# Kernel tuning notes

Hardware: AMD Instinct MI355X
Metric: run time of the kernel (lower is better)

## Reference

```python
import jax, jax.numpy as jnp
import numpy as np

# ---- fixed physiological constants (match init_kwargs cell/synapse params) ----
DT = 0.1  # ms
N_CELL_TYPES = 2
S_REC, S_FF, S_TOT = 3, 1, 4
TAU_MEM = jnp.array([20.0, 10.0])
THETA = jnp.array([-50.0, -50.0])
U_RESET = jnp.array([-65.0, -65.0])
E_L = jnp.array([-70.0, -70.0])
G_L = jnp.array([10.0, 10.0])
TAU_REF_STEPS = jnp.round(jnp.array([2.0, 1.0]) / DT)  # [20, 10] steps
# combined recurrent(3) + FF(1) synapse channels
TAU_RISE = jnp.array([0.5, 2.0, 0.5, 0.5])
TAU_DECAY = jnp.array([2.0, 100.0, 5.0, 2.0])
E_SYN = jnp.array([0.0, 0.0, -80.0, 0.0])
G_BAR = jnp.array([1.0, 0.5, 1.0, 1.0])
SYN2CELL = jnp.array([0, 0, 1])  # recurrent synapse -> presynaptic cell type
A_RISE = jnp.exp(-DT / TAU_RISE)
A_DECAY = jnp.exp(-DT / TAU_DECAY)


def spike(x):
    return (x > 0).astype(x.dtype)


def setup_inputs() -> dict:
    key = jax.random.key(0)
    ks = jax.random.split(key, 8)
    N, NI, B, T = 4096, 1024, 8, 500
    ci = jax.random.randint(ks[0], (N,), 0, 2).astype(jnp.int32)  # 0=exc, 1=inh
    ci_ff = jnp.zeros((NI,), dtype=jnp.int32)
    # sparse signed recurrent weights (Dale's law: sign by presynaptic type)
    mag = jnp.abs(jax.random.normal(ks[1], (N, N))) * 0.02
    sign = jnp.where(ci == 1, -1.0, 1.0)[:, None]
    mask = jax.random.bernoulli(ks[2], 0.1, (N, N))
    weights = (mag * sign * mask).astype(jnp.float32)
    # sparse positive feedforward weights
    mag_ff = jnp.abs(jax.random.normal(ks[3], (NI, N))) * 0.05
    mask_ff = jax.random.bernoulli(ks[4], 0.2, (NI, N))
    weights_FF = (mag_ff * mask_ff).astype(jnp.float32)
    scaling_factors = jax.random.uniform(ks[5], (2, 2), minval=0.5, maxval=1.5)
    scaling_factors_FF = jax.random.uniform(ks[6], (1, 2), minval=0.5, maxval=1.5)
    input_spikes = (jax.random.uniform(ks[7], (B, T, NI)) < 0.05).astype(jnp.float32)
    return {
        "input_spikes": input_spikes,
        "weights": weights,
        "weights_FF": weights_FF,
        "scaling_factors": scaling_factors,
        "scaling_factors_FF": scaling_factors_FF,
        "cell_type_indices": ci,
        "cell_type_indices_FF": ci_ff,
    }


def reference(input_spikes, weights, weights_FF, scaling_factors, scaling_factors_FF,
              cell_type_indices, cell_type_indices_FF):
    ci = cell_type_indices
    B, T, NI = input_spikes.shape
    N = weights.shape[0]
    # per-neuron parameter gathers
    tau_mem = TAU_MEM[ci]
    theta = THETA[ci]
    u_reset = U_RESET[ci]
    e_l = E_L[ci]
    g_l = G_L[ci]
    ref_steps = TAU_REF_STEPS[ci]
    # cell-type pairwise scaling applied to (masked) weights
    W_eff = weights * scaling_factors[ci[:, None], ci[None, :]]            # (N,N)
    Wff_eff = weights_FF * scaling_factors_FF[cell_type_indices_FF[:, None], ci[None, :]]
    cell_masks = jnp.stack([(ci == c).astype(weights.dtype) for c in range(N_CELL_TYPES)])  # (2,N)
    # precompute feedforward synaptic drive for all timesteps: (T,B,N)
    drive_ff = jnp.einsum('bti,ij->tbj', input_spikes, Wff_eff) * G_BAR[S_REC]

    v0 = jnp.broadcast_to(e_l, (B, N))
    h0 = jnp.zeros((B, N, S_TOT), weights.dtype)
    g0 = jnp.zeros((B, N, S_TOT), weights.dtype)
    ref0 = jnp.zeros((B, N), weights.dtype)
    s0 = jnp.zeros((B, N), weights.dtype)

    def step(carry, dff_t):
        v, h, g, ref, s_prev = carry
        # recurrent drive split by presynaptic cell type, routed to synapse channels
        drive_c = jnp.stack([(s_prev * cell_masks[c]) @ W_eff for c in range(N_CELL_TYPES)], axis=-1)  # (B,N,2)
        drive_rec = drive_c[..., SYN2CELL] * G_BAR[:S_REC]                  # (B,N,3)
        drive = jnp.concatenate([drive_rec, dff_t[..., None]], axis=-1)    # (B,N,4)
        # double-exponential conductance kinetics
        h = h * A_RISE + drive
        g = g * A_DECAY + (1.0 - A_DECAY) * h
        # conductance-based membrane update
        I_syn = jnp.sum(g * (E_SYN - v[..., None]), axis=-1)                # (B,N)
        v_new = v + (DT / tau_mem) * ((e_l - v) + I_syn / g_l)
        refr = (ref > 0).astype(v.dtype)
        v_new = refr * u_reset + (1.0 - refr) * v_new
        s_new = spike(v_new - theta) * (1.0 - refr)
        spk = s_new > 0.5
        v_post = jnp.where(spk, u_reset, v_new)
        ref_new = jnp.where(spk, ref_steps, jnp.maximum(ref - 1.0, 0.0))
        return (v_post, h, g, ref_new, s_new), s_new

    _, spikes = jax.lax.scan(step, (v0, h0, g0, ref0, s0), drive_ff)
    return jnp.transpose(spikes, (1, 0, 2))  # (B,T,N)
```

## Files before the change

### kernel.cpp

```cpp
#include <hip/hip_runtime.h>
#include <cstdint>
#include <cstddef>

#define N_NEU   4096
#define N_IN    1024
#define B_SZ    8
#define T_STEPS 500
#define NSLICE  16
#define NBLK    (B_SZ * NSLICE)
#define FF_WORDS (B_SZ * T_STEPS * 16)
#define FFP_STRIDE 33
#define FFP_CAP 128
#define N_PAIRS (B_SZ * T_STEPS)

#define WS_TM_OFF    0
#define WS_MB_OFF    512
#define WS_FFM_OFF   17408
#define WS_FFD_OFF   529408
#define WS_FLN_OFF   66065408
#define WS_FL_OFF    66081792
#define WS_NEED_FFD  (529408 + (size_t)T_STEPS * B_SZ * N_NEU * 4)
#define WS_NEED_FL   (66081792 + (size_t)N_PAIRS * FFP_CAP * 4)

__global__ __launch_bounds__(64) void snn_init(const int* __restrict__ ci,
                                               unsigned long long* __restrict__ tmask,
                                               unsigned long long* __restrict__ mb2) {
    const int k = blockIdx.x, l = threadIdx.x;
    unsigned long long m = __ballot(ci[(k << 6) + l] == 0);
    if (l == 0) tmask[k] = m;
    const int idx = (k << 6) + l;
    if (idx < 2048) mb2[idx] = 0ULL;
}

__global__ __launch_bounds__(256) void snn_ffmask(const float* __restrict__ inspk,
                                                  unsigned long long* __restrict__ ffmask) {
    int gid = blockIdx.x * 256 + threadIdx.x;
    int wid = gid >> 6, lane = gid & 63;
    int nw  = (gridDim.x * 256) >> 6;
    for (int w = wid; w < FF_WORDS; w += nw) {
        float v = inspk[(size_t)w * 64 + lane];
        unsigned long long m = __ballot(v > 0.5f);
        if (lane == 0) ffmask[w] = m;
    }
}

__device__ __forceinline__ int extract_pad(unsigned long long m,
                                           unsigned long long tm_exc,
                                           int* lds, int lane) {
    int pc  = __popcll(m);
    int sum = pc;
#pragma unroll
    for (int d = 1; d < 64; d <<= 1) {
        int o = __shfl_up(sum, d, 64);
        if (lane >= d) sum += o;
    }
    int off   = sum - pc;
    int total = __shfl(sum, 63, 64);
    int base  = lane << 6;
    while (m) {
        int bit = __builtin_ctzll(m);
        int ty  = ((tm_exc >> bit) & 1ULL) ? 0 : 1;
        lds[off++] = ((base + bit) << 2) | ty;
        m &= m - 1ULL;
    }
    int padcnt = (-total) & 63;
    if (lane < padcnt) lds[total + lane] = 2;
    return total;
}

__device__ __forceinline__ int extract_cap(unsigned long long m,
                                           int* buf, int lane) {
    int pc  = __popcll(m);
    int sum = pc;
#pragma unroll
    for (int d = 1; d < 64; d <<= 1) {
        int o = __shfl_up(sum, d, 64);
        if (lane >= d) sum += o;
    }
    int off   = sum - pc;
    int total = __shfl(sum, 63, 64);
    int base  = lane << 6;
    while (m) {
        int bit = __builtin_ctzll(m);
        if (off < FFP_CAP) buf[off] = (base + bit) << 2;
        ++off;
        m &= m - 1ULL;
    }
    if (total < FFP_CAP) {
        int padcnt = (-total) & 63;
        if (lane < padcnt && total + lane < FFP_CAP)
            buf[total + lane] = 2;
    }
    return total;
}

__global__ __launch_bounds__(256) void snn_fflist(
    const unsigned long long* __restrict__ ffmask,
    int* __restrict__ fflist,
    int* __restrict__ fflist_n)
{
    const int lane = threadIdx.x & 63;
    const int wv   = threadIdx.x >> 6;
    const int w    = blockIdx.x * 4 + wv;
    for (int q = 0; q < 4; ++q) {
        const int p = w * 4 + q;
        const int t = p >> 3, b = p & 7;
        const unsigned long long mf =
            (lane < 16) ? ffmask[((size_t)b * T_STEPS + t) * 16 + lane] : 0ULL;
        const int n = extract_cap(mf, fflist + (size_t)p * FFP_CAP, lane);
        if (lane == 0) fflist_n[p] = n;
    }
}

__device__ __forceinline__ void gather2(const int* __restrict__ lst, int npad,
                                        const float* __restrict__ base,
                                        float se, float si,
                                        float* oe, float* oi) {
#pragma clang fp contract(off)
    float ae = 0.0f, ai = 0.0f;
    const int4* lst4 = (const int4*)lst;
    for (int k = 0; k < npad; k += 64) {
        int4  eq[16];
        int   e[64];
        float w[64];
#pragma unroll
        for (int u = 0; u < 16; ++u) eq[u] = lst4[(k >> 2) + u];
#pragma unroll
        for (int u = 0; u < 16; ++u) {
            e[4 * u + 0] = eq[u].x; e[4 * u + 1] = eq[u].y;
            e[4 * u + 2] = eq[u].z; e[4 * u + 3] = eq[u].w;
        }
#pragma unroll
        for (int u = 0; u < 64; ++u) w[u] = base[(size_t)(e[u] >> 2) << 12];
#pragma unroll
        for (int u = 0; u < 64; ++u) {
            const int ty = e[u] & 3;
            const float sc = (ty == 0) ? se : ((ty == 1) ? si : 0.0f);
            const float p  = w[u] * sc;
            ae = (ty == 0) ? ae + p : ae;
            ai = (ty == 1) ? ai + p : ai;
        }
    }
    *oe = ae; *oi = ai;
}

__device__ __forceinline__ float ffp_fold_g(const int* __restrict__ lst, int npad,
                                            const float* __restrict__ lwff,
                                            int j, float sff) {
#pragma clang fp contract(off)
    float acc = 0.0f;
    const int4* l4 = (const int4*)lst;
    for (int k = 0; k < npad; k += 64) {
        int4  eq[16];
        int   e[64];
        float w[64];
#pragma unroll
        for (int u = 0; u < 16; ++u) eq[u] = l4[(k >> 2) + u];
#pragma unroll
        for (int u = 0; u < 16; ++u) {
            e[4 * u + 0] = eq[u].x; e[4 * u + 1] = eq[u].y;
            e[4 * u + 2] = eq[u].z; e[4 * u + 3] = eq[u].w;
        }
#pragma unroll
        for (int u = 0; u < 64; ++u) w[u] = lwff[(e[u] >> 2) * FFP_STRIDE + j];
#pragma unroll
        for (int u = 0; u < 64; ++u) {
            const float sc = ((e[u] & 3) == 0) ? sff : 0.0f;
            const float p  = w[u] * sc;
            acc += p;
        }
    }
    return acc;
}

__global__ __launch_bounds__(512) void snn_ffpre4(
    const unsigned long long* __restrict__ ffmask,
    const float* __restrict__ Wff,
    const float* __restrict__ sfff,
    const int*   __restrict__ ci,
    const int*   __restrict__ fflist,
    const int*   __restrict__ fflist_n,
    float*       __restrict__ ffdrive)
{
#pragma clang fp contract(off)
    const int tid = threadIdx.x;
    const int s   = blockIdx.x & 127;
    const int tbh = blockIdx.x >> 7;
    __shared__ float lwff[N_IN * FFP_STRIDE];

    {
        const int j  = tid & 31;
        const int r0 = tid >> 5;
        for (int r = r0; r < N_IN; r += 16)
            lwff[r * FFP_STRIDE + j] = Wff[(size_t)r * N_NEU + (s << 5) + j];
    }
    __syncthreads();

    const int lane = tid & 63;
    const int wv   = tid >> 6;
    const int j    = lane & 31;
    const int h    = lane >> 5;
    const int jg   = (s << 5) + j;
    const float sff = sfff[ci[jg]];

    for (int k = 0; k < 125; ++k) {
        const int p0 = tbh * 2000 + (((k << 3) | wv) << 1);
        const int p  = p0 + h;
        const int nf = fflist_n[p];
        float acc;
        if (nf <= FFP_CAP) {
            acc = ffp_fold_g(fflist + (size_t)p * FFP_CAP,
                             (nf + 63) & ~63, lwff, j, sff);
        } else {
            const int t = p >> 3, b = p & 7;
            acc = 0.0f;
            const unsigned long long* mp =
                ffmask + ((size_t)b * T_STEPS + t) * 16;
            for (int w16 = 0; w16 < 16; ++w16) {
                unsigned long long mw = mp[w16];
                const int base = w16 << 6;
                while (mw) {
                    const int bit = __builtin_ctzll(mw); mw &= mw - 1ULL;
                    const float pr = lwff[(base + bit) * FFP_STRIDE + j] * sff;
                    acc += pr;
                }
            }
        }
        ffdrive[(size_t)p * N_NEU + jg] = acc;
    }
}

__global__ __launch_bounds__(64) void snn_ffpre(const unsigned long long* __restrict__ ffmask,
                                                const float* __restrict__ Wff,
                                                const float* __restrict__ sfff,
                                                const int*   __restrict__ ci,
                                                float*       __restrict__ ffdrive) {
#pragma clang fp contract(off)
    const int lane  = threadIdx.x;
    const int chunk = blockIdx.x & 63;
    const int tile  = blockIdx.x >> 6;
    const int i     = (chunk << 6) + lane;
    const float s_ff = sfff[ci[i]];
    __shared__ alignas(16) int lds_f[N_IN + 64];
    for (int p = tile * 25; p < tile * 25 + 25; ++p) {
        const int t = p >> 3, b = p & 7;
        const unsigned long long mf =
            (lane < 16) ? ffmask[((size_t)b * T_STEPS + t) * 16 + lane] : 0ULL;
        const int n = extract_pad(mf, ~0ULL, lds_f, lane);
        float fd, dummy;
        gather2(lds_f, (n + 63) & ~63, Wff + i, s_ff, 0.0f, &fd, &dummy);
        ffdrive[((size_t)t * B_SZ + b) * N_NEU + i] = fd;
    }
}

__global__ __launch_bounds__(256) void snn_run(
    const float* __restrict__ W,
    const float* __restrict__ Wff,
    const float* __restrict__ sf,
    const float* __restrict__ sfff,
    const int*   __restrict__ ci,
    float*       __restrict__ out,
    const unsigned long long* __restrict__ ffmask,
    const unsigned long long* __restrict__ tmask_g,
    const float* __restrict__ ffdrive,
    int use_ffpre,
    unsigned long long* __restrict__ mb2)
{
#pragma clang fp contract(off)
    const int tid   = threadIdx.x;
    const int lane  = tid & 63;
    const int wv    = tid >> 6;
    const int bid   = blockIdx.x;
    const int slice = (((bid >> 6) & 1) << 3) | (bid & 7);
    const int b     = (bid >> 3) & 7;
    const int i     = (slice << 8) + (wv << 6) + lane;
    const int c     = ci[i];

    const float s_exc = sf[c];
    const float s_inh = sf[2 + c];
    const float s_ff  = sfff[c];

    const unsigned long long my_tm = tmask_g[lane];

    __shared__ alignas(16) int lds_c[4][N_NEU + 64];
    __shared__ alignas(16) int lds_f[4][N_IN + 64];
    int* const my_ldsc = lds_c[wv];
    int* const my_ldsf = lds_f[wv];

    unsigned long long* const mbB = mb2 + (size_t)b * 128;

    float v = -70.0f, rf = 0.0f;
    float h0 = 0.0f, h1 = 0.0f, h2 = 0.0f, h3 = 0.0f;
    float g0 = 0.0f, g1 = 0.0f, g2 = 0.0f, g3 = 0.0f;

    const float aR0 = expf(-0.1f / 0.5f);
    const float aR1 = expf(-0.1f / 2.0f);
    const float aD0 = expf(-0.1f / 2.0f);
    const float aD1 = expf(-0.1f / 100.0f);
    const float aD2 = expf(-0.1f / 5.0f);
    const float kmem   = c ? (0.1f / 10.0f) : (0.1f / 20.0f);
    const float rsteps = c ? 10.0f : 20.0f;

    const float* const wseg = W + (size_t)((slice << 8) + (wv << 6));

    for (int t = 0; t < T_STEPS; ++t) {
        float ffd = 0.0f;
        if (use_ffpre) {
            ffd = ffdrive[((size_t)t * B_SZ + b) * N_NEU + i];
            asm volatile("" :: "v"(ffd));
        }

        unsigned long long mw = 0ULL;
        if (t > 0) {
            const unsigned int tg = (unsigned int)t;
            const unsigned long long* ep =
                mbB + (size_t)(t & 1) * 1024 + ((size_t)lane << 1);
            unsigned long long w0, w1;
            for (;;) {
                w0 = __hip_atomic_load(&ep[0], __ATOMIC_RELAXED,
                                       __HIP_MEMORY_SCOPE_AGENT);
                w1 = __hip_atomic_load(&ep[1], __ATOMIC_RELAXED,
                                       __HIP_MEMORY_SCOPE_AGENT);
                const bool ok = ((unsigned int)(w0 >> 32) == tg) &&
                                ((unsigned int)(w1 >> 32) == tg);
                if (__ballot(ok) == ~0ULL) break;
                __builtin_amdgcn_s_sleep(1);
            }
            mw = (w0 & 0xFFFFFFFFULL) | ((w1 & 0xFFFFFFFFULL) << 32);
            asm volatile("" ::: "memory");
        }

        {
            unsigned long long mm = mw;
            float wacc = 0.0f;
            const size_t rowbase = (size_t)lane << 18;
            while (mm) {
                const int bit = __builtin_ctzll(mm); mm &= mm - 1ULL;
                const float* r = wseg + rowbase + ((size_t)bit << 12);
                wacc += r[0]; wacc += r[16]; wacc += r[32]; wacc += r[48];
            }
            asm volatile("" :: "v"(wacc));
        }

        int ne = 0;
        if (__ballot(mw != 0ULL) != 0ULL)
            ne = extract_pad(mw, my_tm, my_ldsc, lane);

        if (!use_ffpre) {
            const unsigned long long mf =
                (lane < 16) ? ffmask[((size_t)b * T_STEPS + t) * 16 + lane] : 0ULL;
            const int nf = extract_pad(mf, ~0ULL, my_ldsf, lane);
            float fd, dummy;
            gather2(my_ldsf, (nf + 63) & ~63, Wff + i, s_ff, 0.0f, &fd, &dummy);
            ffd = fd;
        }

        float exc, inh;
        gather2(my_ldsc, (ne + 63) & ~63, W + i, s_exc, s_inh, &exc, &inh);

        const float d0 = exc;
        const float d1 = 0.5f * exc;
        const float d2 = inh;
        const float d3 = ffd;

        h0 = fmaf(h0, aR0, d0);
        h1 = fmaf(h1, aR1, d1);
        h2 = fmaf(h2, aR0, d2);
        h3 = fmaf(h3, aR0, d3);
        g0 = fmaf(g0, aD0, (1.0f - aD0) * h0);
        g1 = fmaf(g1, aD1, (1.0f - aD1) * h1);
        g2 = fmaf(g2, aD2, (1.0f - aD2) * h2);
        g3 = fmaf(g3, aD0, (1.0f - aD0) * h3);

        const float p0 = g0 * (0.0f - v);
        const float p1 = g1 * (0.0f - v);
        const float p2 = g2 * (-80.0f - v);
        const float p3 = g3 * (0.0f - v);
        const float Isyn = ((p0 + p1) + p2) + p3;

        float vn = fmaf(kmem, (-70.0f - v) + Isyn / 10.0f, v);
        const bool refr = rf > 0.0f;
        if (refr) vn = -65.0f;
        const float sn = (!refr && (vn > -50.0f)) ? 1.0f : 0.0f;
        const bool spk = sn > 0.5f;

        const unsigned long long sm = __ballot(spk);
        if (lane == 0) {
            const unsigned long long tg =
                (unsigned long long)(unsigned int)(t + 1) << 32;
            unsigned long long* pp = mb2 + (size_t)((t + 1) & 1) * 1024
                                   + (size_t)b * 128
                                   + ((size_t)((slice << 2) | wv) << 1);
            __hip_atomic_store(&pp[0], tg | (sm & 0xFFFFFFFFULL),
                               __ATOMIC_RELAXED, __HIP_MEMORY_SCOPE_AGENT);
            __hip_atomic_store(&pp[1], tg | (sm >> 32),
                               __ATOMIC_RELAXED, __HIP_MEMORY_SCOPE_AGENT);
        }

        v  = spk ? -65.0f : vn;
        rf = spk ? rsteps : fmaxf(rf - 1.0f, 0.0f);
        out[((size_t)b * T_STEPS + t) * N_NEU + i] = sn;
    }
}

extern "C" void kernel_launch(void* const* d_in, const int* in_sizes, int n_in,
                              void* d_out, int out_size, void* d_ws, size_t ws_size,
                              hipStream_t stream) {
    const float* inspk = (const float*)d_in[0];
    const float* W     = (const float*)d_in[1];
    const float* Wff   = (const float*)d_in[2];
    const float* sf    = (const float*)d_in[3];
    const float* sfff  = (const float*)d_in[4];
    const int*   ci    = (const int*)d_in[5];

    float* out = (float*)d_out;
    unsigned long long* tmask    = (unsigned long long*)((char*)d_ws + WS_TM_OFF);
    unsigned long long* mb2      = (unsigned long long*)((char*)d_ws + WS_MB_OFF);
    unsigned long long* ffmask   = (unsigned long long*)((char*)d_ws + WS_FFM_OFF);
    float*              ffdrive  = (float*)((char*)d_ws + WS_FFD_OFF);
    int*                fflist_n = (int*)((char*)d_ws + WS_FLN_OFF);
    int*                fflist   = (int*)((char*)d_ws + WS_FL_OFF);

    const int use_fl    = (ws_size >= WS_NEED_FL) ? 1 : 0;
    const int use_ffpre = (ws_size >= WS_NEED_FFD) ? 1 : 0;

    snn_init<<<64, 64, 0, stream>>>(ci, tmask, mb2);
    snn_ffmask<<<1000, 256, 0, stream>>>(inspk, ffmask);
    if (use_fl) {
        snn_fflist<<<250, 256, 0, stream>>>(ffmask, fflist, fflist_n);
        snn_ffpre4<<<256, 512, 0, stream>>>(ffmask, Wff, sfff, ci,
                                            fflist, fflist_n, ffdrive);
    } else if (use_ffpre) {
        snn_ffpre<<<160 * 64, 64, 0, stream>>>(ffmask, Wff, sfff, ci, ffdrive);
    }
    snn_run<<<NBLK, 256, 0, stream>>>(W, Wff, sf, sfff, ci, out,
                                      ffmask, tmask, ffdrive, use_ffpre, mb2);
}
```

Measured before the change: 937.0 us.

## Fuse feedforward drive precompute into the recurrent simulation kernel prologue

Removes the separate snn_ffpre4 kernel that staged Wff columns in shared memory. Instead, snn_run is launched with 512 threads, and all eight waves first compute this block's own batch/slice feedforward drive from the spike lists, with the two halves of time split across wave groups. After a barrier the extra four waves exit and the original recurrent loop runs. This saves a kernel launch and reuses the same blocks, but it runs the gather with only 128 blocks reading Wff directly from global memory, and the wider launch bound may change register allocation for the main loop.

```diff
diff --git a/kernel.cpp b/kernel.cpp
--- a/kernel.cpp
+++ b/kernel.cpp
@@ -9,7 +9,6 @@
 #define NSLICE  16
 #define NBLK    (B_SZ * NSLICE)
 #define FF_WORDS (B_SZ * T_STEPS * 16)
-#define FFP_STRIDE 33
 #define FFP_CAP 128
 #define N_PAIRS (B_SZ * T_STEPS)
 
@@ -142,92 +141,6 @@
         }
     }
     *oe = ae; *oi = ai;
-}
-
-__device__ __forceinline__ float ffp_fold_g(const int* __restrict__ lst, int npad,
-                                            const float* __restrict__ lwff,
-                                            int j, float sff) {
-#pragma clang fp contract(off)
-    float acc = 0.0f;
-    const int4* l4 = (const int4*)lst;
-    for (int k = 0; k < npad; k += 64) {
-        int4  eq[16];
-        int   e[64];
-        float w[64];
-#pragma unroll
-        for (int u = 0; u < 16; ++u) eq[u] = l4[(k >> 2) + u];
-#pragma unroll
-        for (int u = 0; u < 16; ++u) {
-            e[4 * u + 0] = eq[u].x; e[4 * u + 1] = eq[u].y;
-            e[4 * u + 2] = eq[u].z; e[4 * u + 3] = eq[u].w;
-        }
-#pragma unroll
-        for (int u = 0; u < 64; ++u) w[u] = lwff[(e[u] >> 2) * FFP_STRIDE + j];
-#pragma unroll
-        for (int u = 0; u < 64; ++u) {
-            const float sc = ((e[u] & 3) == 0) ? sff : 0.0f;
-            const float p  = w[u] * sc;
-            acc += p;
-        }
-    }
-    return acc;
-}
-
-__global__ __launch_bounds__(512) void snn_ffpre4(
-    const unsigned long long* __restrict__ ffmask,
-    const float* __restrict__ Wff,
-    const float* __restrict__ sfff,
-    const int*   __restrict__ ci,
-    const int*   __restrict__ fflist,
-    const int*   __restrict__ fflist_n,
-    float*       __restrict__ ffdrive)
-{
-#pragma clang fp contract(off)
-    const int tid = threadIdx.x;
-    const int s   = blockIdx.x & 127;
-    const int tbh = blockIdx.x >> 7;
-    __shared__ float lwff[N_IN * FFP_STRIDE];
-
-    {
-        const int j  = tid & 31;
-        const int r0 = tid >> 5;
-        for (int r = r0; r < N_IN; r += 16)
-            lwff[r * FFP_STRIDE + j] = Wff[(size_t)r * N_NEU + (s << 5) + j];
-    }
-    __syncthreads();
-
-    const int lane = tid & 63;
-    const int wv   = tid >> 6;
-    const int j    = lane & 31;
-    const int h    = lane >> 5;
-    const int jg   = (s << 5) + j;
-    const float sff = sfff[ci[jg]];
-
-    for (int k = 0; k < 125; ++k) {
-        const int p0 = tbh * 2000 + (((k << 3) | wv) << 1);
-        const int p  = p0 + h;
-        const int nf = fflist_n[p];
-        float acc;
-        if (nf <= FFP_CAP) {
-            acc = ffp_fold_g(fflist + (size_t)p * FFP_CAP,
-                             (nf + 63) & ~63, lwff, j, sff);
-        } else {
-            const int t = p >> 3, b = p & 7;
-            acc = 0.0f;
-            const unsigned long long* mp =
-                ffmask + ((size_t)b * T_STEPS + t) * 16;
-            for (int w16 = 0; w16 < 16; ++w16) {
-                unsigned long long mw = mp[w16];
-                const int base = w16 << 6;
-                while (mw) {
-                    const int bit = __builtin_ctzll(mw); mw &= mw - 1ULL;
-                    const float pr = lwff[(base + bit) * FFP_STRIDE + j] * sff;
-                    acc += pr;
-                }
-            }
-        }
-        ffdrive[(size_t)p * N_NEU + jg] = acc;
-    }
 }
 
 __global__ __launch_bounds__(64) void snn_ffpre(const unsigned long long* __restrict__ ffmask,
@@ -253,7 +166,7 @@
     }
 }
 
-__global__ __launch_bounds__(256) void snn_run(
+__global__ __launch_bounds__(512) void snn_run(
     const float* __restrict__ W,
     const float* __restrict__ Wff,
     const float* __restrict__ sf,
@@ -262,8 +175,11 @@
     float*       __restrict__ out,
     const unsigned long long* __restrict__ ffmask,
     const unsigned long long* __restrict__ tmask_g,
-    const float* __restrict__ ffdrive,
+    float*       __restrict__ ffdrive,
+    const int*   __restrict__ fflist,
+    const int*   __restrict__ fflist_n,
     int use_ffpre,
+    int use_fl,
     unsigned long long* __restrict__ mb2)
 {
 #pragma clang fp contract(off)
@@ -273,8 +189,42 @@
     const int bid   = blockIdx.x;
     const int slice = (((bid >> 6) & 1) << 3) | (bid & 7);
     const int b     = (bid >> 3) & 7;
-    const int i     = (slice << 8) + (wv << 6) + lane;
-    const int c     = ci[i];
+
+    if (use_fl) {
+        const int pwv = wv & 3;
+        const int ii  = (slice << 8) + (pwv << 6) + lane;
+        const float psff = sfff[ci[ii]];
+        const int t0 = (wv >> 2) ? 250 : 0;
+        for (int t = t0; t < t0 + 250; ++t) {
+            const int p  = (t << 3) | b;
+            const int nf = fflist_n[p];
+            float fd, dummy;
+            if (nf <= FFP_CAP) {
+                gather2(fflist + (size_t)p * FFP_CAP, (nf + 63) & ~63,
+                        Wff + ii, psff, 0.0f, &fd, &dummy);
+            } else {
+                fd = 0.0f;
+                const unsigned long long* mp =
+                    ffmask + ((size_t)b * T_STEPS + t) * 16;
+                for (int w16 = 0; w16 < 16; ++w16) {
+                    unsigned long long mw = mp[w16];
+                    const int base = w16 << 6;
+                    while (mw) {
+                        const int bit = __builtin_ctzll(mw); mw &= mw - 1ULL;
+                        const float pr =
+                            Wff[((size_t)(base + bit) << 12) + ii] * psff;
+                        fd += pr;
+                    }
+                }
+            }
+            ffdrive[(size_t)p * N_NEU + ii] = fd;
+        }
+    }
+    __syncthreads();
+    if (wv >= 4) return;
+
+    const int i = (slice << 8) + (wv << 6) + lane;
+    const int c = ci[i];
 
     const float s_exc = sf[c];
     const float s_inh = sf[2 + c];
@@ -428,11 +378,11 @@
     snn_ffmask<<<1000, 256, 0, stream>>>(inspk, ffmask);
     if (use_fl) {
         snn_fflist<<<250, 256, 0, stream>>>(ffmask, fflist, fflist_n);
-        snn_ffpre4<<<256, 512, 0, stream>>>(ffmask, Wff, sfff, ci,
-                                            fflist, fflist_n, ffdrive);
     } else if (use_ffpre) {
         snn_ffpre<<<160 * 64, 64, 0, stream>>>(ffmask, Wff, sfff, ci, ffdrive);
     }
-    snn_run<<<NBLK, 256, 0, stream>>>(W, Wff, sf, sfff, ci, out,
-                                      ffmask, tmask, ffdrive, use_ffpre, mb2);
-}
+    snn_run<<<NBLK, 512, 0, stream>>>(W, Wff, sf, sfff, ci, out,
+                                      ffmask, tmask, ffdrive,
+                                      fflist, fflist_n,
+                                      use_ffpre, use_fl, mb2);
+}
```

After: 1.394 ms. 1.49x slower.
